# Optimization experiments

Measured on AMD Instinct MI355X. Metric: run time of the kernel, lower is better.

Reference implementation:

```python
import jax, jax.numpy as jnp
import numpy as np

N_NODES = 100000   # vertices
N_EDGES = 20000    # hyperedges
NNZ = 1600000      # incidence entries (avg vertex degree 16)
D_IN = 128
D_OUT = 128


def setup_inputs() -> dict:
    key = jax.random.key(0)
    k1, k2, k3, k4, k5 = jax.random.split(key, 5)
    X = jax.random.normal(k1, (N_NODES, D_IN), dtype=jnp.float32)
    v_idx = jax.random.randint(k2, (NNZ,), 0, N_NODES)
    e_idx = jax.random.randint(k3, (NNZ,), 0, N_EDGES)
    theta_w = jax.random.normal(k4, (D_IN, D_OUT), dtype=jnp.float32) / np.sqrt(D_IN)
    theta_b = jax.random.normal(k5, (D_OUT,), dtype=jnp.float32) * 0.01
    return {"X": X, "theta_w": theta_w, "theta_b": theta_b,
            "v_idx": v_idx, "e_idx": e_idx}


def reference(X, theta_w, theta_b, v_idx, e_idx):
    # degrees (edge weights w_e = 1)
    ones = jnp.ones(v_idx.shape[0], dtype=X.dtype)
    d_v = jax.ops.segment_sum(ones, v_idx, num_segments=N_NODES)   # [N]
    d_e = jax.ops.segment_sum(ones, e_idx, num_segments=N_EDGES)   # [M]
    inv_sqrt_dv = jnp.where(d_v > 0, d_v ** -0.5, 0.0)
    inv_de = jnp.where(d_e > 0, 1.0 / d_e, 0.0)

    # theta: dense GEMM
    Xt = X @ theta_w + theta_b                                     # [N, D_OUT]

    # smoothing_with_HGNN: D_v^{-1/2} H W D_e^{-1} H^T D_v^{-1/2} Xt
    Xs = Xt * inv_sqrt_dv[:, None]                                 # [N, D_OUT]
    Ye = jax.ops.segment_sum(Xs[v_idx], e_idx, num_segments=N_EDGES)  # H^T Xs -> [M, D_OUT]
    Ye = Ye * inv_de[:, None]
    Xv = jax.ops.segment_sum(Ye[e_idx], v_idx, num_segments=N_NODES)  # H Ye -> [N, D_OUT]
    return jax.nn.relu(Xv * inv_sqrt_dv[:, None])
```

## Files before the change

kernel.cpp:

```cpp
#include <hip/hip_runtime.h>

#define N_NODES 100000
#define N_EDGES 20000
#define NNZ     1600000
#define D       128
#define DW      64

#define NB      256
#define CAP_E   8192
#define CAP_V   8192
#define SPAN_E  ((N_EDGES + NB - 1) / NB)
#define SPAN_V  ((N_NODES + NB - 1) / NB)
#define P1_CHUNK 8192
#define P1_ITER  (P1_CHUNK / 256)
#define P1_BLOCKS ((NNZ + P1_CHUNK - 1) / P1_CHUNK)

typedef __attribute__((ext_vector_type(8))) short bf16x8;
typedef __attribute__((ext_vector_type(4))) float f32x4;

__device__ __forceinline__ unsigned int pack_bf2(float lo, float hi) {
  unsigned int ul = __float_as_uint(lo), uh = __float_as_uint(hi);
  ul = (ul + 0x7FFFu + ((ul >> 16) & 1u)) >> 16;
  uh = (uh + 0x7FFFu + ((uh >> 16) & 1u)) & 0xFFFF0000u;
  return ul | uh;
}

__global__ void k_zero_cursors(int* __restrict__ cur) {
  cur[threadIdx.x] = 0;
}

__global__ __launch_bounds__(256) void k_bin(const int* __restrict__ v_idx, const int* __restrict__ e_idx,
                                             int* __restrict__ ce, int* __restrict__ cv,
                                             unsigned int* __restrict__ Te, unsigned int* __restrict__ Tv) {
  __shared__ int he[NB], hv[NB], be[NB], bv[NB], le[NB], lv[NB];
  int t = threadIdx.x;
  he[t] = 0; hv[t] = 0; le[t] = 0; lv[t] = 0;
  __syncthreads();
  int base = blockIdx.x * P1_CHUNK;
  int v[P1_ITER], e[P1_ITER];
#pragma unroll
  for (int j = 0; j < P1_ITER; ++j) {
    int idx = base + j * 256 + t;
    if (idx < NNZ) {
      v[j] = v_idx[idx]; e[j] = e_idx[idx];
      atomicAdd(&he[e[j] / SPAN_E], 1);
      atomicAdd(&hv[v[j] / SPAN_V], 1);
    } else v[j] = -1;
  }
  __syncthreads();
  be[t] = he[t] ? atomicAdd(&ce[t], he[t]) : 0;
  bv[t] = hv[t] ? atomicAdd(&cv[t], hv[t]) : 0;
  __syncthreads();
#pragma unroll
  for (int j = 0; j < P1_ITER; ++j) {
    if (v[j] < 0) continue;
    int eb = e[j] / SPAN_E, vb = v[j] / SPAN_V;
    int se = be[eb] + atomicAdd(&le[eb], 1);
    int sv = bv[vb] + atomicAdd(&lv[vb], 1);
    if (se < CAP_E) Te[(size_t)eb * CAP_E + se] = ((unsigned)e[j] << 17) | (unsigned)v[j];
    if (sv < CAP_V) Tv[(size_t)vb * CAP_V + sv] = ((unsigned)v[j] << 15) | (unsigned)e[j];
  }
}

__global__ __launch_bounds__(256) void k_sort(const int* __restrict__ ce, const int* __restrict__ cv,
                                              unsigned int* __restrict__ Te, unsigned int* __restrict__ Tv,
                                              int* __restrict__ cnt_e, float* __restrict__ invde,
                                              int* __restrict__ starts_e,
                                              int* __restrict__ cnt_v, float* __restrict__ risv,
                                              int* __restrict__ starts_v,
                                              const float* __restrict__ X, unsigned int* __restrict__ Xs,
                                              const float* __restrict__ W, unsigned int* __restrict__ Wtp,
                                              unsigned int* __restrict__ Yeb) {
  __shared__ unsigned int raw[CAP_V];
  __shared__ int hist[SPAN_V], lcur[SPAN_V], loff[SPAN_V + 1];
  __shared__ int sd[256];
  __shared__ float rv[SPAN_V];
  int t = threadIdx.x;
  if (blockIdx.x >= 2 * NB) {
    int bp = blockIdx.x - 2 * NB;
    if (bp == 0) {
      if (t < DW) { Xs[(size_t)N_NODES * DW + t] = 0u; Yeb[(size_t)N_EDGES * DW + t] = 0u; }
      if (t == 0) risv[N_NODES] = 0.f;
    }
    int idx = bp * 256 + t;
    if (idx < D * DW) {
      int c = idx & 127, kp = idx >> 7;
      float lo = W[(size_t)(2 * kp) * D + c];
      float hi = W[(size_t)(2 * kp + 1) * D + c];
      Wtp[c * DW + kp] = pack_bf2(lo, hi);
    }
    return;
  }
  if (blockIdx.x < NB) {
    int b = blockIdx.x;
    int v0 = b * SPAN_V;
    int span = N_NODES - v0; if (span > SPAN_V) span = SPAN_V;
    if (span <= 0) return;
    int n = cv[b]; if (n > CAP_V) n = CAP_V; if (n < 0) n = 0;
    for (int i = t; i < n; i += 256) raw[i] = Tv[(size_t)b * CAP_V + i];
    for (int i = t; i < span; i += 256) { hist[i] = 0; lcur[i] = 0; }
    __syncthreads();
    for (int i = t; i < n; i += 256) atomicAdd(&hist[(int)(raw[i] >> 15) - v0], 1);
    __syncthreads();
    {
      int i0 = 2 * t, i1 = 2 * t + 1;
      int s0 = (i0 < span) ? hist[i0] : 0;
      int s1 = (i1 < span) ? hist[i1] : 0;
      int mysum = s0 + s1;
      sd[t] = mysum; __syncthreads();
      for (int off = 1; off < 256; off <<= 1) {
        int add = (t >= off) ? sd[t - off] : 0;
        __syncthreads(); sd[t] += add; __syncthreads();
      }
      int bse = sd[t] - mysum;
      if (i0 < span) loff[i0] = bse;
      if (i1 < span) loff[i1] = bse + s0;
      __syncthreads();
    }
    for (int i = t; i < n; i += 256) {
      unsigned int p = raw[i];
      int l = (int)(p >> 15) - v0;
      int slot = loff[l] + atomicAdd(&lcur[l], 1);
      Tv[(size_t)b * CAP_V + slot] = p & 0x7FFFu;
    }
    for (int i = t; i < span; i += 256) {
      int d = hist[i];
      float r = d > 0 ? rsqrtf((float)d) : 0.0f;
      cnt_v[v0 + i] = d;
      risv[v0 + i] = r;
      rv[i] = r;
      starts_v[v0 + i] = b * CAP_V + loff[i];
    }
    __syncthreads();
    int total = span * DW;
    for (int idx = t; idx < total; idx += 256) {
      int vl = idx >> 6;
      float r = rv[vl];
      size_t gp = (size_t)(v0 + vl) * DW + (idx & 63);
      float2 x = *(const float2*)(X + gp * 2);
      Xs[gp] = pack_bf2(r * x.x, r * x.y);
    }
  } else {
    int b = blockIdx.x - NB;
    int e0 = b * SPAN_E;
    int span = N_EDGES - e0; if (span > SPAN_E) span = SPAN_E;
    if (span <= 0) return;
    int n = ce[b]; if (n > CAP_E) n = CAP_E; if (n < 0) n = 0;
    for (int i = t; i < n; i += 256) raw[i] = Te[(size_t)b * CAP_E + i];
    for (int i = t; i < span; i += 256) { hist[i] = 0; lcur[i] = 0; }
    __syncthreads();
    for (int i = t; i < n; i += 256) atomicAdd(&hist[(int)(raw[i] >> 17) - e0], 1);
    __syncthreads();
    {
      int i0 = 2 * t, i1 = 2 * t + 1;
      int s0 = (i0 < span) ? hist[i0] : 0;
      int s1 = (i1 < span) ? hist[i1] : 0;
      int mysum = s0 + s1;
      sd[t] = mysum; __syncthreads();
      for (int off = 1; off < 256; off <<= 1) {
        int add = (t >= off) ? sd[t - off] : 0;
        __syncthreads(); sd[t] += add; __syncthreads();
      }
      int bse = sd[t] - mysum;
      if (i0 < span) loff[i0] = bse;
      if (i1 < span) loff[i1] = bse + s0;
      __syncthreads();
    }
    for (int i = t; i < n; i += 256) {
      unsigned int p = raw[i];
      int l = (int)(p >> 17) - e0;
      int slot = loff[l] + atomicAdd(&lcur[l], 1);
      Te[(size_t)b * CAP_E + slot] = p & 0x1FFFFu;
    }
    for (int i = t; i < span; i += 256) {
      int d = hist[i];
      cnt_e[e0 + i] = d;
      invde[e0 + i] = d > 0 ? 1.0f / (float)d : 0.0f;
      starts_e[e0 + i] = b * CAP_E + loff[i];
    }
  }
}

__global__ __launch_bounds__(256) void k_eg_gemm(const unsigned int* __restrict__ Xs, const float* __restrict__ risv,
                                                 const int* __restrict__ starts_e, const int* __restrict__ cnt_e,
                                                 const unsigned int* __restrict__ members,
                                                 const unsigned int* __restrict__ Wtp, const float* __restrict__ bias,
                                                 const float* __restrict__ invde, unsigned short* __restrict__ Yeb) {
  __shared__ unsigned int Qls[16][DW];
  __shared__ float qls[16], ivls[16];
  int tid = threadIdx.x;
  int wv = tid >> 6, lane = tid & 63;
  int g = lane >> 4, l16 = lane & 15;
  int row = wv * 4 + g;
  int e = blockIdx.x * 16 + row;
  int beg = starts_e[e];
  int cnt = cnt_e[e];
  int maxc = cnt;
  maxc = max(maxc, __shfl_xor(maxc, 16));
  maxc = max(maxc, __shfl_xor(maxc, 32));
  float a0=0,a1=0,a2=0,a3=0,a4=0,a5=0,a6=0,a7=0,q=0.f;
  for (int i = 0; i < maxc; i += 8) {
    int vv[8];
#pragma unroll
    for (int j = 0; j < 8; ++j) {
      int idx = i + j;
      int m = (int)members[beg + idx];
      vv[j] = (idx < cnt) ? m : N_NODES;
    }
    uint4 xx[8];
#pragma unroll
    for (int j = 0; j < 8; ++j) xx[j] = *(const uint4*)(Xs + (size_t)vv[j] * DW + l16 * 4);
#pragma unroll
    for (int j = 0; j < 8; ++j) q += risv[vv[j]];
#pragma unroll
    for (int j = 0; j < 8; ++j) {
      a0 += __uint_as_float(xx[j].x << 16); a1 += __uint_as_float(xx[j].x & 0xFFFF0000u);
      a2 += __uint_as_float(xx[j].y << 16); a3 += __uint_as_float(xx[j].y & 0xFFFF0000u);
      a4 += __uint_as_float(xx[j].z << 16); a5 += __uint_as_float(xx[j].z & 0xFFFF0000u);
      a6 += __uint_as_float(xx[j].w << 16); a7 += __uint_as_float(xx[j].w & 0xFFFF0000u);
    }
  }
  uint4 o;
  o.x = pack_bf2(a0, a1); o.y = pack_bf2(a2, a3);
  o.z = pack_bf2(a4, a5); o.w = pack_bf2(a6, a7);
  *(uint4*)&Qls[row][(l16 ^ row) * 4] = o;
  if (l16 == 0) { qls[row] = q; ivls[row] = invde[e]; }
  __syncthreads();
  f32x4 acc[2];
  acc[0] = (f32x4){0.f,0.f,0.f,0.f}; acc[1] = (f32x4){0.f,0.f,0.f,0.f};
#pragma unroll
  for (int kt = 0; kt < 4; ++kt) {
    int s = kt * 4 + g;
    bf16x8 a = *(const bf16x8*)&Qls[l16][(s ^ l16) * 4];
#pragma unroll
    for (int n = 0; n < 2; ++n) {
      int nt = wv * 2 + n;
      bf16x8 b = *(const bf16x8*)(Wtp + (size_t)(nt * 16 + l16) * DW + kt * 16 + g * 4);
      acc[n] = __builtin_amdgcn_mfma_f32_16x16x32_bf16(a, b, acc[n], 0, 0, 0);
    }
  }
#pragma unroll
  for (int r = 0; r < 4; ++r) {
    int lrow = g * 4 + r;
    int erow = blockIdx.x * 16 + lrow;
    float s = ivls[lrow], qq = qls[lrow];
#pragma unroll
    for (int n = 0; n < 2; ++n) {
      int c = (wv * 2 + n) * 16 + l16;
      float val = s * (acc[n][r] + qq * bias[c]);
      unsigned int u = __float_as_uint(val);
      u = (u + 0x7FFFu + ((u >> 16) & 1u)) >> 16;
      Yeb[(size_t)erow * D + c] = (unsigned short)u;
    }
  }
}

__global__ __launch_bounds__(256) void k_vertex_gather(const unsigned int* __restrict__ Yeb, const float* __restrict__ risv,
                                const int* __restrict__ starts_v, const int* __restrict__ cnt_v,
                                const unsigned int* __restrict__ members,
                                float* __restrict__ out) {
  int wv = (blockIdx.x * 256 + threadIdx.x) >> 6;
  int lane = threadIdx.x & 63;
  int g = lane >> 4, l16 = lane & 15;
  int v = wv * 4 + g;
  if (v >= N_NODES) return;
  int beg = starts_v[v];
  int cnt = cnt_v[v];
  int maxc = cnt;
  maxc = max(maxc, __shfl_xor(maxc, 16));
  maxc = max(maxc, __shfl_xor(maxc, 32));
  float a0=0,a1=0,a2=0,a3=0,a4=0,a5=0,a6=0,a7=0;
  for (int i = 0; i < maxc; i += 8) {
    int ee[8];
#pragma unroll
    for (int j = 0; j < 8; ++j) {
      int idx = i + j;
      int m = (int)members[beg + idx];
      ee[j] = (idx < cnt) ? m : N_EDGES;
    }
    uint4 yy[8];
#pragma unroll
    for (int j = 0; j < 8; ++j) yy[j] = *(const uint4*)(Yeb + (size_t)ee[j] * DW + l16 * 4);
#pragma unroll
    for (int j = 0; j < 8; ++j) {
      a0 += __uint_as_float(yy[j].x << 16); a1 += __uint_as_float(yy[j].x & 0xFFFF0000u);
      a2 += __uint_as_float(yy[j].y << 16); a3 += __uint_as_float(yy[j].y & 0xFFFF0000u);
      a4 += __uint_as_float(yy[j].z << 16); a5 += __uint_as_float(yy[j].z & 0xFFFF0000u);
      a6 += __uint_as_float(yy[j].w << 16); a7 += __uint_as_float(yy[j].w & 0xFFFF0000u);
    }
  }
  float s = risv[v];
  float4 o0, o1;
  o0.x = fmaxf(a0 * s, 0.f); o0.y = fmaxf(a1 * s, 0.f);
  o0.z = fmaxf(a2 * s, 0.f); o0.w = fmaxf(a3 * s, 0.f);
  o1.x = fmaxf(a4 * s, 0.f); o1.y = fmaxf(a5 * s, 0.f);
  o1.z = fmaxf(a6 * s, 0.f); o1.w = fmaxf(a7 * s, 0.f);
  float* orow = out + (size_t)v * D + l16 * 8;
  *(float4*)orow = o0;
  *(float4*)(orow + 4) = o1;
}

extern "C" void kernel_launch(void* const* d_in, const int* in_sizes, int n_in,
                              void* d_out, int out_size, void* d_ws, size_t ws_size,
                              hipStream_t stream) {
  const float* X    = (const float*)d_in[0];
  const float* W    = (const float*)d_in[1];
  const float* bias = (const float*)d_in[2];
  const int* v_idx  = (const int*)d_in[3];
  const int* e_idx  = (const int*)d_in[4];
  float* out = (float*)d_out;

  char* p = (char*)d_ws;
  auto alloc = [&](size_t bytes) { char* r = p; p += (bytes + 255) & ~(size_t)255; return r; };
  unsigned int* Te  = (unsigned int*)alloc(((size_t)NB + 1) * CAP_E * 4);
  unsigned int* Tv  = (unsigned int*)alloc(((size_t)NB + 1) * CAP_V * 4);
  unsigned int* Xs  = (unsigned int*)alloc((size_t)(N_NODES + 1) * DW * 4);
  unsigned int* Yeb = (unsigned int*)alloc((size_t)(N_EDGES + 1) * DW * 4);
  unsigned int* Wtp = (unsigned int*)alloc((size_t)D * DW * 4);
  float* risv  = (float*)alloc((size_t)(N_NODES + 1) * 4);
  float* invde = (float*)alloc((size_t)N_EDGES * 4);
  int* cnt_e    = (int*)alloc((size_t)N_EDGES * 4);
  int* cnt_v    = (int*)alloc((size_t)N_NODES * 4);
  int* starts_e = (int*)alloc((size_t)N_EDGES * 4);
  int* starts_v = (int*)alloc((size_t)N_NODES * 4);
  int* cursors  = (int*)alloc((size_t)2 * NB * 4);
  int* ce = cursors, *cv = cursors + NB;

  k_zero_cursors<<<1, 2 * NB, 0, stream>>>(cursors);
  k_bin<<<P1_BLOCKS, 256, 0, stream>>>(v_idx, e_idx, ce, cv, Te, Tv);
  k_sort<<<2 * NB + 32, 256, 0, stream>>>(ce, cv, Te, Tv, cnt_e, invde, starts_e,
                                          cnt_v, risv, starts_v, X, Xs, W, Wtp, Yeb);
  k_eg_gemm<<<N_EDGES / 16, 256, 0, stream>>>(Xs, risv, starts_e, cnt_e, Te, Wtp, bias, invde,
                                              (unsigned short*)Yeb);
  k_vertex_gather<<<(N_NODES / 4 + 3) / 4, 256, 0, stream>>>(Yeb, risv, starts_v, cnt_v, Tv, out);
}
```

Measured before the change: 268.2 us.

## Split hyperedge gather into vertex-range slices for cache locality, then reduce and GEMM

The k_sort pass now sorts each hyperedge's member list by vertex slice (8 slices of the node range) and records per-slice counts. A new k_egA kernel gathers Xs rows per (edge group, slice) block, so concurrently running blocks touch a narrower vertex range and reuse L2 better. It also gives 8x more blocks for parallelism. A second kernel, k_gemm2, reduces the 8 partial sums and runs the MFMA GEMM. In exchange it adds a partial-sum buffer round trip, an extra launch, and bf16 rounding of the partials, and the counts are packed into 8 bits per slice, which could overflow on high-degree edges.

```diff
diff --git a/kernel.cpp b/kernel.cpp
--- a/kernel.cpp
+++ b/kernel.cpp
@@ -5,12 +5,15 @@
 #define NNZ     1600000
 #define D       128
 #define DW      64
+#define NSLICE  8
+#define VSLICE  (N_NODES / NSLICE)
 
 #define NB      256
 #define CAP_E   8192
 #define CAP_V   8192
 #define SPAN_E  ((N_EDGES + NB - 1) / NB)
 #define SPAN_V  ((N_NODES + NB - 1) / NB)
+#define SP8     (SPAN_E * NSLICE)
 #define P1_CHUNK 8192
 #define P1_ITER  (P1_CHUNK / 256)
 #define P1_BLOCKS ((NNZ + P1_CHUNK - 1) / P1_CHUNK)
@@ -65,14 +68,14 @@
 __global__ __launch_bounds__(256) void k_sort(const int* __restrict__ ce, const int* __restrict__ cv,
                                               unsigned int* __restrict__ Te, unsigned int* __restrict__ Tv,
                                               int* __restrict__ cnt_e, float* __restrict__ invde,
-                                              int* __restrict__ starts_e,
+                                              int* __restrict__ starts_e, uint2* __restrict__ cnt_es,
                                               int* __restrict__ cnt_v, float* __restrict__ risv,
                                               int* __restrict__ starts_v,
                                               const float* __restrict__ X, unsigned int* __restrict__ Xs,
                                               const float* __restrict__ W, unsigned int* __restrict__ Wtp,
                                               unsigned int* __restrict__ Yeb) {
   __shared__ unsigned int raw[CAP_V];
-  __shared__ int hist[SPAN_V], lcur[SPAN_V], loff[SPAN_V + 1];
+  __shared__ int hist[SP8], lcur[SP8], loff[SP8 + 1];
   __shared__ int sd[256];
   __shared__ float rv[SPAN_V];
   int t = threadIdx.x;
@@ -145,38 +148,162 @@
     int e0 = b * SPAN_E;
     int span = N_EDGES - e0; if (span > SPAN_E) span = SPAN_E;
     if (span <= 0) return;
+    int sp8 = span * NSLICE;
     int n = ce[b]; if (n > CAP_E) n = CAP_E; if (n < 0) n = 0;
     for (int i = t; i < n; i += 256) raw[i] = Te[(size_t)b * CAP_E + i];
-    for (int i = t; i < span; i += 256) { hist[i] = 0; lcur[i] = 0; }
+    for (int i = t; i < sp8; i += 256) { hist[i] = 0; lcur[i] = 0; }
     __syncthreads();
-    for (int i = t; i < n; i += 256) atomicAdd(&hist[(int)(raw[i] >> 17) - e0], 1);
+    for (int i = t; i < n; i += 256) {
+      unsigned int p = raw[i];
+      int l = (int)(p >> 17) - e0;
+      int s = (int)(p & 0x1FFFFu) / VSLICE;
+      atomicAdd(&hist[l * NSLICE + s], 1);
+    }
     __syncthreads();
     {
-      int i0 = 2 * t, i1 = 2 * t + 1;
-      int s0 = (i0 < span) ? hist[i0] : 0;
-      int s1 = (i1 < span) ? hist[i1] : 0;
-      int mysum = s0 + s1;
+      int i0 = 3 * t;
+      int s0 = (i0 < sp8) ? hist[i0] : 0;
+      int s1 = (i0 + 1 < sp8) ? hist[i0 + 1] : 0;
+      int s2 = (i0 + 2 < sp8) ? hist[i0 + 2] : 0;
+      int mysum = s0 + s1 + s2;
       sd[t] = mysum; __syncthreads();
       for (int off = 1; off < 256; off <<= 1) {
         int add = (t >= off) ? sd[t - off] : 0;
         __syncthreads(); sd[t] += add; __syncthreads();
       }
       int bse = sd[t] - mysum;
-      if (i0 < span) loff[i0] = bse;
-      if (i1 < span) loff[i1] = bse + s0;
+      if (i0 < sp8)     loff[i0]     = bse;
+      if (i0 + 1 < sp8) loff[i0 + 1] = bse + s0;
+      if (i0 + 2 < sp8) loff[i0 + 2] = bse + s0 + s1;
       __syncthreads();
     }
     for (int i = t; i < n; i += 256) {
       unsigned int p = raw[i];
       int l = (int)(p >> 17) - e0;
-      int slot = loff[l] + atomicAdd(&lcur[l], 1);
-      Te[(size_t)b * CAP_E + slot] = p & 0x1FFFFu;
+      unsigned v = p & 0x1FFFFu;
+      int k2 = l * NSLICE + (int)v / VSLICE;
+      int slot = loff[k2] + atomicAdd(&lcur[k2], 1);
+      Te[(size_t)b * CAP_E + slot] = v;
     }
     for (int i = t; i < span; i += 256) {
-      int d = hist[i];
+      int c0 = hist[i*8+0], c1 = hist[i*8+1], c2 = hist[i*8+2], c3 = hist[i*8+3];
+      int c4 = hist[i*8+4], c5 = hist[i*8+5], c6 = hist[i*8+6], c7 = hist[i*8+7];
+      int d = c0+c1+c2+c3+c4+c5+c6+c7;
       cnt_e[e0 + i] = d;
       invde[e0 + i] = d > 0 ? 1.0f / (float)d : 0.0f;
-      starts_e[e0 + i] = b * CAP_E + loff[i];
+      starts_e[e0 + i] = b * CAP_E + loff[i * NSLICE];
+      cnt_es[e0 + i] = make_uint2((unsigned)(c0|(c1<<8)|(c2<<16)|(c3<<24)),
+                                  (unsigned)(c4|(c5<<8)|(c6<<16)|(c7<<24)));
+    }
+  }
+}
+
+__global__ __launch_bounds__(256) void k_egA(const unsigned int* __restrict__ Xs, const float* __restrict__ risv,
+                                             const int* __restrict__ starts_e, const uint2* __restrict__ cnt_es,
+                                             const unsigned int* __restrict__ members,
+                                             unsigned int* __restrict__ Qp, float* __restrict__ qp) {
+  int slice = blockIdx.x & 7;
+  int grp = blockIdx.x >> 3;
+  int tid = threadIdx.x;
+  int wv = tid >> 6, lane = tid & 63;
+  int g = lane >> 4, l16 = lane & 15;
+  int row = wv * 4 + g;
+  int e = grp * 16 + row;
+  uint2 cs = cnt_es[e];
+  int c[8];
+  c[0]=cs.x&255; c[1]=(cs.x>>8)&255; c[2]=(cs.x>>16)&255; c[3]=(cs.x>>24)&255;
+  c[4]=cs.y&255; c[5]=(cs.y>>8)&255; c[6]=(cs.y>>16)&255; c[7]=(cs.y>>24)&255;
+  int pre = 0;
+  for (int s = 0; s < slice; ++s) pre += c[s];
+  int len = c[slice];
+  int beg = starts_e[e] + pre;
+  int maxc = len;
+  maxc = max(maxc, __shfl_xor(maxc, 16));
+  maxc = max(maxc, __shfl_xor(maxc, 32));
+  float a0=0,a1=0,a2=0,a3=0,a4=0,a5=0,a6=0,a7=0,q=0.f;
+  for (int i = 0; i < maxc; i += 4) {
+    int vv[4];
+#pragma unroll
+    for (int j = 0; j < 4; ++j) {
+      int idx = i + j;
+      int m = (int)members[beg + idx];
+      vv[j] = (idx < len) ? m : N_NODES;
+    }
+    uint4 xx[4];
+#pragma unroll
+    for (int j = 0; j < 4; ++j) xx[j] = *(const uint4*)(Xs + (size_t)vv[j] * DW + l16 * 4);
+#pragma unroll
+    for (int j = 0; j < 4; ++j) q += risv[vv[j]];
+#pragma unroll
+    for (int j = 0; j < 4; ++j) {
+      a0 += __uint_as_float(xx[j].x << 16); a1 += __uint_as_float(xx[j].x & 0xFFFF0000u);
+      a2 += __uint_as_float(xx[j].y << 16); a3 += __uint_as_float(xx[j].y & 0xFFFF0000u);
+      a4 += __uint_as_float(xx[j].z << 16); a5 += __uint_as_float(xx[j].z & 0xFFFF0000u);
+      a6 += __uint_as_float(xx[j].w << 16); a7 += __uint_as_float(xx[j].w & 0xFFFF0000u);
+    }
+  }
+  uint4 o;
+  o.x = pack_bf2(a0, a1); o.y = pack_bf2(a2, a3);
+  o.z = pack_bf2(a4, a5); o.w = pack_bf2(a6, a7);
+  *(uint4*)(Qp + ((size_t)e * NSLICE + slice) * DW + l16 * 4) = o;
+  if (l16 == 0) qp[(size_t)e * NSLICE + slice] = q;
+}
+
+__global__ __launch_bounds__(256) void k_gemm2(const unsigned int* __restrict__ Qp, const float* __restrict__ qp,
+                                               const unsigned int* __restrict__ Wtp, const float* __restrict__ bias,
+                                               const float* __restrict__ invde, unsigned short* __restrict__ Yeb) {
+  __shared__ unsigned int Qls[16][DW];
+  __shared__ float qls[16], ivls[16];
+  int tid = threadIdx.x;
+  int wv = tid >> 6, lane = tid & 63;
+  int g = lane >> 4, l16 = lane & 15;
+  int row = wv * 4 + g;
+  int e = blockIdx.x * 16 + row;
+  float a0=0,a1=0,a2=0,a3=0,a4=0,a5=0,a6=0,a7=0;
+#pragma unroll
+  for (int s = 0; s < NSLICE; ++s) {
+    uint4 x = *(const uint4*)(Qp + ((size_t)e * NSLICE + s) * DW + l16 * 4);
+    a0 += __uint_as_float(x.x << 16); a1 += __uint_as_float(x.x & 0xFFFF0000u);
+    a2 += __uint_as_float(x.y << 16); a3 += __uint_as_float(x.y & 0xFFFF0000u);
+    a4 += __uint_as_float(x.z << 16); a5 += __uint_as_float(x.z & 0xFFFF0000u);
+    a6 += __uint_as_float(x.w << 16); a7 += __uint_as_float(x.w & 0xFFFF0000u);
+  }
+  uint4 o;
+  o.x = pack_bf2(a0, a1); o.y = pack_bf2(a2, a3);
+  o.z = pack_bf2(a4, a5); o.w = pack_bf2(a6, a7);
+  *(uint4*)&Qls[row][(l16 ^ row) * 4] = o;
+  if (l16 == 0) {
+    float q = 0.f;
+#pragma unroll
+    for (int s = 0; s < NSLICE; ++s) q += qp[(size_t)e * NSLICE + s];
+    qls[row] = q; ivls[row] = invde[e];
+  }
+  __syncthreads();
+  f32x4 acc[2];
+  acc[0] = (f32x4){0.f,0.f,0.f,0.f}; acc[1] = (f32x4){0.f,0.f,0.f,0.f};
+#pragma unroll
+  for (int kt = 0; kt < 4; ++kt) {
+    int s = kt * 4 + g;
+    bf16x8 a = *(const bf16x8*)&Qls[l16][(s ^ l16) * 4];
+#pragma unroll
+    for (int n = 0; n < 2; ++n) {
+      int nt = wv * 2 + n;
+      bf16x8 b = *(const bf16x8*)(Wtp + (size_t)(nt * 16 + l16) * DW + kt * 16 + g * 4);
+      acc[n] = __builtin_amdgcn_mfma_f32_16x16x32_bf16(a, b, acc[n], 0, 0, 0);
+    }
+  }
+#pragma unroll
+  for (int r = 0; r < 4; ++r) {
+    int lrow = g * 4 + r;
+    int erow = blockIdx.x * 16 + lrow;
+    float s = ivls[lrow], qq = qls[lrow];
+#pragma unroll
+    for (int n = 0; n < 2; ++n) {
+      int cc = (wv * 2 + n) * 16 + l16;
+      float val = s * (acc[n][r] + qq * bias[cc]);
+      unsigned int u = __float_as_uint(val);
+      u = (u + 0x7FFFu + ((u >> 16) & 1u)) >> 16;
+      Yeb[(size_t)erow * D + cc] = (unsigned short)u;
     }
   }
 }
@@ -246,11 +373,11 @@
     float s = ivls[lrow], qq = qls[lrow];
 #pragma unroll
     for (int n = 0; n < 2; ++n) {
-      int c = (wv * 2 + n) * 16 + l16;
-      float val = s * (acc[n][r] + qq * bias[c]);
+      int cc = (wv * 2 + n) * 16 + l16;
+      float val = s * (acc[n][r] + qq * bias[cc]);
       unsigned int u = __float_as_uint(val);
       u = (u + 0x7FFFu + ((u >> 16) & 1u)) >> 16;
-      Yeb[(size_t)erow * D + c] = (unsigned short)u;
+      Yeb[(size_t)erow * D + cc] = (unsigned short)u;
     }
   }
 }
@@ -320,17 +447,27 @@
   float* risv  = (float*)alloc((size_t)(N_NODES + 1) * 4);
   float* invde = (float*)alloc((size_t)N_EDGES * 4);
   int* cnt_e    = (int*)alloc((size_t)N_EDGES * 4);
+  uint2* cnt_es = (uint2*)alloc((size_t)N_EDGES * 8);
   int* cnt_v    = (int*)alloc((size_t)N_NODES * 4);
   int* starts_e = (int*)alloc((size_t)N_EDGES * 4);
   int* starts_v = (int*)alloc((size_t)N_NODES * 4);
   int* cursors  = (int*)alloc((size_t)2 * NB * 4);
   int* ce = cursors, *cv = cursors + NB;
+  unsigned int* Qp = (unsigned int*)alloc((size_t)N_EDGES * NSLICE * DW * 4);
+  float* qp        = (float*)alloc((size_t)N_EDGES * NSLICE * 4);
+  size_t need = (size_t)(p - (char*)d_ws);
+  bool sliced = ws_size >= need;
 
   k_zero_cursors<<<1, 2 * NB, 0, stream>>>(cursors);
   k_bin<<<P1_BLOCKS, 256, 0, stream>>>(v_idx, e_idx, ce, cv, Te, Tv);
-  k_sort<<<2 * NB + 32, 256, 0, stream>>>(ce, cv, Te, Tv, cnt_e, invde, starts_e,
+  k_sort<<<2 * NB + 32, 256, 0, stream>>>(ce, cv, Te, Tv, cnt_e, invde, starts_e, cnt_es,
                                           cnt_v, risv, starts_v, X, Xs, W, Wtp, Yeb);
-  k_eg_gemm<<<N_EDGES / 16, 256, 0, stream>>>(Xs, risv, starts_e, cnt_e, Te, Wtp, bias, invde,
-                                              (unsigned short*)Yeb);
+  if (sliced) {
+    k_egA<<<NSLICE * (N_EDGES / 16), 256, 0, stream>>>(Xs, risv, starts_e, cnt_es, Te, Qp, qp);
+    k_gemm2<<<N_EDGES / 16, 256, 0, stream>>>(Qp, qp, Wtp, bias, invde, (unsigned short*)Yeb);
+  } else {
+    k_eg_gemm<<<N_EDGES / 16, 256, 0, stream>>>(Xs, risv, starts_e, cnt_e, Te, Wtp, bias, invde,
+                                                (unsigned short*)Yeb);
+  }
   k_vertex_gather<<<(N_NODES / 4 + 3) / 4, 256, 0, stream>>>(Yeb, risv, starts_v, cnt_v, Tv, out);
 }
```

Result: faster. 262.5 us (-2.1%).
